# Kernel optimization log

Measured on AMD Instinct MI355X. Metric: run time of the kernel, lower is better.

Reference implementation:

```python
import jax, jax.numpy as jnp
import numpy as np

B, L, D = 2, 2048, 1024
H = 16          # num_heads == num_key_value_heads
FD = 16         # feature_dim (q/k head dim)
HD = D // H     # head_dim = 64 (v head dim)
EPS = 1e-5


def setup_inputs() -> dict:
    key = jax.random.key(0)
    k0, k1, k2, k3, k4 = jax.random.split(key, 5)
    scale = 0.02
    return {
        "hidden_states": jax.random.normal(k0, (B, L, D), jnp.float32),
        "Wq": jax.random.normal(k1, (D, H * FD), jnp.float32) * scale,
        "Wk": jax.random.normal(k2, (D, H * FD), jnp.float32) * scale,
        "Wv": jax.random.normal(k3, (D, H * HD), jnp.float32) * scale,
        "Wo": jax.random.normal(k4, (H * HD, D), jnp.float32) * scale,
    }


def reference(hidden_states, Wq, Wk, Wv, Wo):
    # projections (bias-free), split heads: b l (h d) -> b h l d
    q = (hidden_states @ Wq).reshape(B, L, H, FD).transpose(0, 2, 1, 3)
    k = (hidden_states @ Wk).reshape(B, L, H, FD).transpose(0, 2, 1, 3)
    v = (hidden_states @ Wv).reshape(B, L, H, HD).transpose(0, 2, 1, 3)

    # parallel_rebased: squared-dot-product kernel attention, causal,
    # row-normalized by the kernel sum (use_scale=True, use_normalize=True)
    qk_scale = FD ** -0.5
    s = jnp.einsum('bhqd,bhkd->bhqk', q * qk_scale, k)
    s = s * s  # quadratic feature map: (q.k)^2
    causal = jnp.tril(jnp.ones((L, L), dtype=bool))
    s = jnp.where(causal, s, 0.0)
    z = jnp.sum(s, axis=-1)  # [B,H,L]
    o = jnp.einsum('bhqk,bhkd->bhqd', s, v) / (z[..., None] + EPS)

    # merge heads: b h l d -> b l (h d), output projection
    o = o.transpose(0, 2, 1, 3).reshape(B, L, H * HD)
    return o @ Wo
```

## Files before the change

kernel.cpp:

```cpp
#include <hip/hip_runtime.h>
#include <hip/hip_bf16.h>

#define BB 2
#define LL 2048
#define DD 1024
#define HH 16
#define FD 16
#define HD 64
#define EPS 1e-5f
#define RQKV 1536
#define NFIX 4

typedef __attribute__((ext_vector_type(4))) float f32x4;
typedef __attribute__((ext_vector_type(8))) _Float16 f16x8;
typedef __attribute__((ext_vector_type(4))) _Float16 f16x4;

__global__ __launch_bounds__(256) void transpose_cast(
    const float* __restrict__ src, _Float16* __restrict__ dst, int K, int N) {
  __shared__ _Float16 s[32][40];
  const int n0 = blockIdx.x * 32, k0 = blockIdx.y * 32;
  const int tid = threadIdx.x;
  {
    int r = tid >> 3, c = (tid & 7) * 4;
    float4 v = *(const float4*)(src + (size_t)(k0 + r) * N + n0 + c);
    f16x4 p = {(_Float16)v.x, (_Float16)v.y, (_Float16)v.z, (_Float16)v.w};
    *(f16x4*)&s[r][c] = p;
  }
  __syncthreads();
  {
    int n = tid >> 3, kk = (tid & 7) * 4;
    f16x4 o = {s[kk + 0][n], s[kk + 1][n], s[kk + 2][n], s[kk + 3][n]};
    *(f16x4*)(dst + (size_t)(n0 + n) * K + k0 + kk) = o;
  }
}

template <typename AT, typename OutT>
__global__ __launch_bounds__(256) void gemm_tn(
    const AT* __restrict__ A, const _Float16* __restrict__ Bt,
    OutT* __restrict__ C, int M, int N, int K) {
  constexpr int LDT = 40;
  __shared__ __attribute__((aligned(16))) _Float16 sA[128 * LDT];
  __shared__ __attribute__((aligned(16))) _Float16 sB[128 * LDT];
  const int tid = threadIdx.x;
  const int m0 = blockIdx.y * 128, n0 = blockIdx.x * 128;
  const int w = tid >> 6, lane = tid & 63, quad = lane >> 4, l16 = lane & 15;
  const int wm = (w >> 1) * 64, wn = (w & 1) * 64;

  const int sr = tid >> 1, sh = (tid & 1) * 16;
  const AT* Ag = A + (size_t)(m0 + sr) * K + sh;
  const _Float16* Bg = Bt + (size_t)(n0 + sr) * K + sh;
  _Float16* sAw = &sA[sr * LDT + sh];
  _Float16* sBw = &sB[sr * LDT + sh];

  f32x4 acc[4][4];
#pragma unroll
  for (int i = 0; i < 4; i++)
#pragma unroll
    for (int j = 0; j < 4; j++) acc[i][j] = (f32x4){0.f, 0.f, 0.f, 0.f};

  float4 ar32[4];
  f16x8 ar16[2];
  f16x8 br[2];
  auto LOAD = [&](int k0) {
    if constexpr (sizeof(AT) == 4) {
      ar32[0] = *(const float4*)(Ag + k0);
      ar32[1] = *(const float4*)(Ag + k0 + 4);
      ar32[2] = *(const float4*)(Ag + k0 + 8);
      ar32[3] = *(const float4*)(Ag + k0 + 12);
    } else {
      ar16[0] = *(const f16x8*)(Ag + k0);
      ar16[1] = *(const f16x8*)(Ag + k0 + 8);
    }
    br[0] = *(const f16x8*)(Bg + k0);
    br[1] = *(const f16x8*)(Bg + k0 + 8);
  };
  LOAD(0);

  for (int k0 = 0; k0 < K; k0 += 32) {
    __syncthreads();
    if constexpr (sizeof(AT) == 4) {
      f16x8 p0 = {(_Float16)ar32[0].x, (_Float16)ar32[0].y, (_Float16)ar32[0].z, (_Float16)ar32[0].w,
                  (_Float16)ar32[1].x, (_Float16)ar32[1].y, (_Float16)ar32[1].z, (_Float16)ar32[1].w};
      f16x8 p1 = {(_Float16)ar32[2].x, (_Float16)ar32[2].y, (_Float16)ar32[2].z, (_Float16)ar32[2].w,
                  (_Float16)ar32[3].x, (_Float16)ar32[3].y, (_Float16)ar32[3].z, (_Float16)ar32[3].w};
      *(f16x8*)sAw = p0;
      *(f16x8*)(sAw + 8) = p1;
    } else {
      *(f16x8*)sAw = ar16[0];
      *(f16x8*)(sAw + 8) = ar16[1];
    }
    *(f16x8*)sBw = br[0];
    *(f16x8*)(sBw + 8) = br[1];
    __syncthreads();
    if (k0 + 32 < K) LOAD(k0 + 32);

    f16x8 af[4], bf[4];
#pragma unroll
    for (int i = 0; i < 4; i++)
      af[i] = *(const f16x8*)&sA[(wm + i * 16 + l16) * LDT + quad * 8];
#pragma unroll
    for (int j = 0; j < 4; j++)
      bf[j] = *(const f16x8*)&sB[(wn + j * 16 + l16) * LDT + quad * 8];
#pragma unroll
    for (int i = 0; i < 4; i++)
#pragma unroll
      for (int j = 0; j < 4; j++)
        acc[i][j] = __builtin_amdgcn_mfma_f32_16x16x32_f16(af[i], bf[j], acc[i][j], 0, 0, 0);
  }

#pragma unroll
  for (int i = 0; i < 4; i++)
#pragma unroll
    for (int j = 0; j < 4; j++)
#pragma unroll
      for (int r = 0; r < 4; r++) {
        const int row = m0 + wm + i * 16 + quad * 4 + r;
        const int col = n0 + wn + j * 16 + l16;
        C[(size_t)row * N + col] = (OutT)acc[i][j][r];
      }
}

#define SK4 24
#define SV4 88
#define SS4 88

__global__ __launch_bounds__(256) void attn_mfma4(
    const _Float16* __restrict__ QKV, _Float16* __restrict__ O) {
  __shared__ __attribute__((aligned(16))) _Float16 sK[64 * SK4];
  __shared__ __attribute__((aligned(16))) _Float16 sVt[80 * SV4];
  __shared__ __attribute__((aligned(16))) _Float16 sS2[4 * 32 * SS4];

  const int bh = blockIdx.y;
  const int b = bh >> 4, h = bh & 15;
  const int qtA = blockIdx.x;
  const int qtB = 31 - qtA;
  const int tid = threadIdx.x;
  const int w = tid >> 6;
  const int lane = tid & 63;
  const int quad = lane >> 4;
  const int l16 = lane & 15;
  const int gqA = qtA * 64 + w * 16;
  const int gqB = qtB * 64 + w * 16;

  f16x8 qfragA = {}, qfragB = {};
  if (quad < 2) {
    qfragA = *(const f16x8*)(QKV +
        (size_t)(b * LL + gqA + l16) * RQKV + h * FD + quad * 8);
    qfragB = *(const f16x8*)(QKV +
        (size_t)(b * LL + gqB + l16) * RQKV + h * FD + quad * 8);
  }

  for (int t = tid; t < 16 * SV4; t += 256) {
    int r = t / SV4, c = t % SV4;
    sVt[64 * SV4 + t] = (_Float16)((r == 0 && c < 64) ? 1.0f : 0.0f);
  }
  __syncthreads();
  const f16x8 zf0 = *(const f16x8*)&sVt[(64 + l16) * SV4 + quad * 8];
  const f16x8 zf1 = *(const f16x8*)&sVt[(64 + l16) * SV4 + 32 + quad * 8];

  f32x4 oaccA[4], oaccB[4];
  f32x4 zaccA = (f32x4){0.f, 0.f, 0.f, 0.f};
  f32x4 zaccB = (f32x4){0.f, 0.f, 0.f, 0.f};
#pragma unroll
  for (int nt = 0; nt < 4; nt++) {
    oaccA[nt] = (f32x4){0.f, 0.f, 0.f, 0.f};
    oaccB[nt] = (f32x4){0.f, 0.f, 0.f, 0.f};
  }

  _Float16* sS2B = sS2 + w * 32 * SS4;
  _Float16* sS2A = sS2B + 16 * SS4;

  const int ktiles = qtB + 1;

  const int skey = tid >> 2, sfg = (tid & 3) * 4;
  uint2 kreg;
  f16x8 vreg0, vreg1;
  auto LOAD = [&](int kt) {
    kreg = *(const uint2*)(QKV +
        (size_t)(b * LL + kt * 64 + skey) * RQKV + 256 + h * FD + sfg);
    const _Float16* vp = QKV +
        (size_t)(b * LL + kt * 64 + lane) * RQKV + 512 + h * HD + w * 16;
    vreg0 = *(const f16x8*)vp;
    vreg1 = *(const f16x8*)(vp + 8);
  };
  LOAD(0);

  for (int kt = 0; kt < ktiles; kt++) {
    __syncthreads();
    *(uint2*)&sK[skey * SK4 + sfg] = kreg;
#pragma unroll
    for (int t = 0; t < 8; t++) sVt[(w * 16 + t) * SV4 + lane] = vreg0[t];
#pragma unroll
    for (int t = 0; t < 8; t++) sVt[(w * 16 + 8 + t) * SV4 + lane] = vreg1[t];
    __syncthreads();
    if (kt + 1 < ktiles) LOAD(kt + 1);

    const int k0 = kt * 64;
    const bool activeA = (kt <= qtA);

    f16x8 kf[4];
#pragma unroll
    for (int nt = 0; nt < 4; nt++) {
      f16x8 f = {};
      if (quad < 2) f = *(const f16x8*)&sK[(nt * 16 + l16) * SK4 + quad * 8];
      kf[nt] = f;
    }

    {
      const bool mask = (kt == qtB);
#pragma unroll
      for (int nt = 0; nt < 4; nt++) {
        f32x4 s = __builtin_amdgcn_mfma_f32_16x16x32_f16(
            qfragB, kf[nt], (f32x4){0.f, 0.f, 0.f, 0.f}, 0, 0, 0);
        const int gk = k0 + nt * 16 + l16;
#pragma unroll
        for (int r = 0; r < 4; r++) {
          float sv = s[r] * s[r] * 2.0f;
          if (mask) sv = (gk <= gqB + quad * 4 + r) ? sv : 0.0f;
          sS2B[(quad * 4 + r) * SS4 + nt * 16 + l16] = (_Float16)sv;
        }
      }
    }
    if (activeA) {
      const bool mask = (kt == qtA);
#pragma unroll
      for (int nt = 0; nt < 4; nt++) {
        f32x4 s = __builtin_amdgcn_mfma_f32_16x16x32_f16(
            qfragA, kf[nt], (f32x4){0.f, 0.f, 0.f, 0.f}, 0, 0, 0);
        const int gk = k0 + nt * 16 + l16;
#pragma unroll
        for (int r = 0; r < 4; r++) {
          float sv = s[r] * s[r] * 2.0f;
          if (mask) sv = (gk <= gqA + quad * 4 + r) ? sv : 0.0f;
          sS2A[(quad * 4 + r) * SS4 + nt * 16 + l16] = (_Float16)sv;
        }
      }
    }
    __asm__ volatile("s_waitcnt lgkmcnt(0)" ::: "memory");

    f16x8 afB0 = *(const f16x8*)&sS2B[l16 * SS4 + quad * 8];
    f16x8 afB1 = *(const f16x8*)&sS2B[l16 * SS4 + 32 + quad * 8];
    f16x8 afA0 = {}, afA1 = {};
    if (activeA) {
      afA0 = *(const f16x8*)&sS2A[l16 * SS4 + quad * 8];
      afA1 = *(const f16x8*)&sS2A[l16 * SS4 + 32 + quad * 8];
    }

#pragma unroll
    for (int nt = 0; nt < 4; nt++) {
      f16x8 vf0 = *(const f16x8*)&sVt[(nt * 16 + l16) * SV4 + quad * 8];
      f16x8 vf1 = *(const f16x8*)&sVt[(nt * 16 + l16) * SV4 + 32 + quad * 8];
      oaccB[nt] = __builtin_amdgcn_mfma_f32_16x16x32_f16(afB0, vf0, oaccB[nt], 0, 0, 0);
      oaccB[nt] = __builtin_amdgcn_mfma_f32_16x16x32_f16(afB1, vf1, oaccB[nt], 0, 0, 0);
      if (activeA) {
        oaccA[nt] = __builtin_amdgcn_mfma_f32_16x16x32_f16(afA0, vf0, oaccA[nt], 0, 0, 0);
        oaccA[nt] = __builtin_amdgcn_mfma_f32_16x16x32_f16(afA1, vf1, oaccA[nt], 0, 0, 0);
      }
    }
    zaccB = __builtin_amdgcn_mfma_f32_16x16x32_f16(afB0, zf0, zaccB, 0, 0, 0);
    zaccB = __builtin_amdgcn_mfma_f32_16x16x32_f16(afB1, zf1, zaccB, 0, 0, 0);
    if (activeA) {
      zaccA = __builtin_amdgcn_mfma_f32_16x16x32_f16(afA0, zf0, zaccA, 0, 0, 0);
      zaccA = __builtin_amdgcn_mfma_f32_16x16x32_f16(afA1, zf1, zaccA, 0, 0, 0);
    }
  }

  {
    float rz[4];
#pragma unroll
    for (int r = 0; r < 4; r++) {
      float zz = __shfl(zaccB[r], lane & 48);
      rz[r] = 1.0f / (zz + 32.0f * EPS);
    }
#pragma unroll
    for (int nt = 0; nt < 4; nt++)
#pragma unroll
      for (int r = 0; r < 4; r++) {
        const int gq = gqB + quad * 4 + r;
        O[(size_t)(b * LL + gq) * (HH * HD) + h * HD + nt * 16 + l16] =
            (_Float16)(oaccB[nt][r] * rz[r]);
      }
  }
  {
    float rz[4];
#pragma unroll
    for (int r = 0; r < 4; r++) {
      float zz = __shfl(zaccA[r], lane & 48);
      rz[r] = 1.0f / (zz + 32.0f * EPS);
    }
#pragma unroll
    for (int nt = 0; nt < 4; nt++)
#pragma unroll
      for (int r = 0; r < 4; r++) {
        const int gq = gqA + quad * 4 + r;
        O[(size_t)(b * LL + gq) * (HH * HD) + h * HD + nt * 16 + l16] =
            (_Float16)(oaccA[nt][r] * rz[r]);
      }
  }
}

__global__ __launch_bounds__(256) void early_qkv(
    const float* __restrict__ hs, const float* __restrict__ Wq,
    const float* __restrict__ Wk, const float* __restrict__ Wv,
    float* __restrict__ QKVe) {
  __shared__ float sHS[8][DD];
  __shared__ float part[8][8][32];
  const int tid = threadIdx.x;
  const int kg = tid >> 5, c = tid & 31;
  const int c0 = blockIdx.x * 32;

  for (int i = tid; i < 8 * (DD / 4); i += 256) {
    int e = i / (DD / 4), col4 = (i % (DD / 4)) * 4;
    int b = e >> 2, r = e & 3;
    *(float4*)&sHS[e][col4] =
        *(const float4*)(hs + (size_t)(b * LL + r) * DD + col4);
  }
  __syncthreads();

  const float* W;
  int col, ncol;
  if (c0 < 256) { W = Wq; col = c0 + c; ncol = 256; }
  else if (c0 < 512) { W = Wk; col = (c0 - 256) + c; ncol = 256; }
  else { W = Wv; col = (c0 - 512) + c; ncol = 1024; }

  float acc[8] = {};
  const int d0 = kg * 128;
#pragma unroll 4
  for (int d = d0; d < d0 + 128; d++) {
    float wv = W[(size_t)d * ncol + col];
#pragma unroll
    for (int e = 0; e < 8; e++) acc[e] += sHS[e][d] * wv;
  }
#pragma unroll
  for (int e = 0; e < 8; e++) part[kg][e][c] = acc[e];
  __syncthreads();

  {
    int e = tid >> 5;
    float t = 0.f;
#pragma unroll
    for (int g = 0; g < 8; g++) t += part[g][e][c];
    QKVe[(size_t)e * RQKV + c0 + c] = t;
  }
}

__global__ __launch_bounds__(256) void fix_final(
    const float* __restrict__ QKVe, _Float16* __restrict__ Oatt) {
  const int b = blockIdx.x >> 4, h = blockIdx.x & 15;
  const int tid = threadIdx.x;
  const int p = tid >> 6, d = tid & 63;

  float num = 0.f, z = 0.f;
  const float* qrow = QKVe + (size_t)(b * 4 + p) * RQKV + h * FD;
  for (int j = 0; j <= p; j++) {
    const float* krow = QKVe + (size_t)(b * 4 + j) * RQKV + 256 + h * FD;
    float s = 0.f;
#pragma unroll
    for (int f = 0; f < FD; f++) s += qrow[f] * krow[f];
    s *= 0.25f;
    s = s * s;
    z += s;
    num += s * QKVe[(size_t)(b * 4 + j) * RQKV + 512 + h * HD + d];
  }
  Oatt[(size_t)(b * LL + p) * (HH * HD) + h * HD + d] =
      (_Float16)(num / (z + EPS));
}

extern "C" void kernel_launch(void* const* d_in, const int* in_sizes, int n_in,
                              void* d_out, int out_size, void* d_ws, size_t ws_size,
                              hipStream_t stream) {
  const float* hs = (const float*)d_in[0];
  const float* Wq = (const float*)d_in[1];
  const float* Wk = (const float*)d_in[2];
  const float* Wv = (const float*)d_in[3];
  const float* Wo = (const float*)d_in[4];
  float* out = (float*)d_out;

  char* ws = (char*)d_ws;
  _Float16* WqkvT = (_Float16*)ws;
  _Float16* WoT   = (_Float16*)(ws + (3ull << 20));
  _Float16* QKV   = (_Float16*)(ws + (8ull << 20));
  _Float16* Oatt  = (_Float16*)(ws + (20ull << 20));
  float*    QKVe  = (float*)(ws + (28ull << 20));

  const int M = BB * LL;

  transpose_cast<<<dim3(256 / 32, DD / 32), 256, 0, stream>>>(Wq, WqkvT, DD, 256);
  transpose_cast<<<dim3(256 / 32, DD / 32), 256, 0, stream>>>(Wk, WqkvT + 256 * DD, DD, 256);
  transpose_cast<<<dim3(DD / 32, DD / 32), 256, 0, stream>>>(Wv, WqkvT + 512 * DD, DD, DD);
  transpose_cast<<<dim3(DD / 32, DD / 32), 256, 0, stream>>>(Wo, WoT, DD, DD);

  early_qkv<<<dim3(RQKV / 32), 256, 0, stream>>>(hs, Wq, Wk, Wv, QKVe);

  gemm_tn<float, _Float16><<<dim3(RQKV / 128, M / 128), 256, 0, stream>>>(
      hs, WqkvT, QKV, M, RQKV, DD);

  attn_mfma4<<<dim3(LL / 128, BB * HH), 256, 0, stream>>>(QKV, Oatt);

  fix_final<<<dim3(BB * HH), 256, 0, stream>>>(QKVe, Oatt);

  gemm_tn<_Float16, float><<<dim3(DD / 128, M / 128), 256, 0, stream>>>(
      Oatt, WoT, out, M, DD, DD);
}
```

Before: 189.0 us.

## Pre-cast hidden states to fp16, merge QKV weight transposes, deepen GEMM K-tile to 64

Adds a separate kernel that converts hidden_states to fp16 once, so the QKV GEMM reads half-width input instead of converting fp32 inside its main loop. The three Q/K/V weight transpose launches are merged into one kernel. The GEMM K-tile grows from 32 to 64, with padded shared-memory rows, which halves the number of loop iterations and barriers. The cost is an extra pass over the activations and about twice the shared memory per block, which may reduce occupancy.

```diff
diff --git a/kernel.cpp b/kernel.cpp
--- a/kernel.cpp
+++ b/kernel.cpp
@@ -15,6 +15,46 @@
 typedef __attribute__((ext_vector_type(8))) _Float16 f16x8;
 typedef __attribute__((ext_vector_type(4))) _Float16 f16x4;
 
+__global__ __launch_bounds__(256) void cast_hs(
+    const float* __restrict__ src, _Float16* __restrict__ dst, int n) {
+  int idx = (blockIdx.x * 256 + threadIdx.x) * 16;
+  if (idx >= n) return;
+#pragma unroll
+  for (int half = 0; half < 2; half++) {
+    float4 a = *(const float4*)(src + idx + half * 8);
+    float4 b = *(const float4*)(src + idx + half * 8 + 4);
+    f16x8 p = {(_Float16)a.x, (_Float16)a.y, (_Float16)a.z, (_Float16)a.w,
+               (_Float16)b.x, (_Float16)b.y, (_Float16)b.z, (_Float16)b.w};
+    *(f16x8*)(dst + idx + half * 8) = p;
+  }
+}
+
+__global__ __launch_bounds__(256) void transpose_qkv(
+    const float* __restrict__ Wq, const float* __restrict__ Wk,
+    const float* __restrict__ Wv, _Float16* __restrict__ dst) {
+  __shared__ _Float16 s[32][40];
+  const int ct = blockIdx.x % 48, kt = blockIdx.x / 48;
+  const float* src;
+  int n0, ncol, drow;
+  if (ct < 8) { src = Wq; n0 = ct * 32; ncol = 256; drow = n0; }
+  else if (ct < 16) { src = Wk; n0 = (ct - 8) * 32; ncol = 256; drow = 256 + n0; }
+  else { src = Wv; n0 = (ct - 16) * 32; ncol = 1024; drow = 512 + n0; }
+  const int k0 = kt * 32;
+  const int tid = threadIdx.x;
+  {
+    int r = tid >> 3, c = (tid & 7) * 4;
+    float4 v = *(const float4*)(src + (size_t)(k0 + r) * ncol + n0 + c);
+    f16x4 p = {(_Float16)v.x, (_Float16)v.y, (_Float16)v.z, (_Float16)v.w};
+    *(f16x4*)&s[r][c] = p;
+  }
+  __syncthreads();
+  {
+    int n = tid >> 3, kk = (tid & 7) * 4;
+    f16x4 o = {s[kk + 0][n], s[kk + 1][n], s[kk + 2][n], s[kk + 3][n]};
+    *(f16x4*)(dst + (size_t)(drow + n) * DD + k0 + kk) = o;
+  }
+}
+
 __global__ __launch_bounds__(256) void transpose_cast(
     const float* __restrict__ src, _Float16* __restrict__ dst, int K, int N) {
   __shared__ _Float16 s[32][40];
@@ -34,11 +74,11 @@
   }
 }
 
-template <typename AT, typename OutT>
-__global__ __launch_bounds__(256) void gemm_tn(
-    const AT* __restrict__ A, const _Float16* __restrict__ Bt,
+template <typename OutT>
+__global__ __launch_bounds__(256) void gemm_f16(
+    const _Float16* __restrict__ A, const _Float16* __restrict__ Bt,
     OutT* __restrict__ C, int M, int N, int K) {
-  constexpr int LDT = 40;
+  constexpr int LDT = 72;
   __shared__ __attribute__((aligned(16))) _Float16 sA[128 * LDT];
   __shared__ __attribute__((aligned(16))) _Float16 sB[128 * LDT];
   const int tid = threadIdx.x;
@@ -46,8 +86,8 @@
   const int w = tid >> 6, lane = tid & 63, quad = lane >> 4, l16 = lane & 15;
   const int wm = (w >> 1) * 64, wn = (w & 1) * 64;
 
-  const int sr = tid >> 1, sh = (tid & 1) * 16;
-  const AT* Ag = A + (size_t)(m0 + sr) * K + sh;
+  const int sr = tid >> 1, sh = (tid & 1) * 32;
+  const _Float16* Ag = A + (size_t)(m0 + sr) * K + sh;
   const _Float16* Bg = Bt + (size_t)(n0 + sr) * K + sh;
   _Float16* sAw = &sA[sr * LDT + sh];
   _Float16* sBw = &sB[sr * LDT + sh];
@@ -58,54 +98,41 @@
 #pragma unroll
     for (int j = 0; j < 4; j++) acc[i][j] = (f32x4){0.f, 0.f, 0.f, 0.f};
 
-  float4 ar32[4];
-  f16x8 ar16[2];
-  f16x8 br[2];
+  f16x8 ar[4], br[4];
   auto LOAD = [&](int k0) {
-    if constexpr (sizeof(AT) == 4) {
-      ar32[0] = *(const float4*)(Ag + k0);
-      ar32[1] = *(const float4*)(Ag + k0 + 4);
-      ar32[2] = *(const float4*)(Ag + k0 + 8);
-      ar32[3] = *(const float4*)(Ag + k0 + 12);
-    } else {
-      ar16[0] = *(const f16x8*)(Ag + k0);
-      ar16[1] = *(const f16x8*)(Ag + k0 + 8);
-    }
-    br[0] = *(const f16x8*)(Bg + k0);
-    br[1] = *(const f16x8*)(Bg + k0 + 8);
+#pragma unroll
+    for (int i = 0; i < 4; i++) {
+      ar[i] = *(const f16x8*)(Ag + k0 + i * 8);
+      br[i] = *(const f16x8*)(Bg + k0 + i * 8);
+    }
   };
   LOAD(0);
 
-  for (int k0 = 0; k0 < K; k0 += 32) {
+  for (int k0 = 0; k0 < K; k0 += 64) {
     __syncthreads();
-    if constexpr (sizeof(AT) == 4) {
-      f16x8 p0 = {(_Float16)ar32[0].x, (_Float16)ar32[0].y, (_Float16)ar32[0].z, (_Float16)ar32[0].w,
-                  (_Float16)ar32[1].x, (_Float16)ar32[1].y, (_Float16)ar32[1].z, (_Float16)ar32[1].w};
-      f16x8 p1 = {(_Float16)ar32[2].x, (_Float16)ar32[2].y, (_Float16)ar32[2].z, (_Float16)ar32[2].w,
-                  (_Float16)ar32[3].x, (_Float16)ar32[3].y, (_Float16)ar32[3].z, (_Float16)ar32[3].w};
-      *(f16x8*)sAw = p0;
-      *(f16x8*)(sAw + 8) = p1;
-    } else {
-      *(f16x8*)sAw = ar16[0];
-      *(f16x8*)(sAw + 8) = ar16[1];
-    }
-    *(f16x8*)sBw = br[0];
-    *(f16x8*)(sBw + 8) = br[1];
+#pragma unroll
+    for (int i = 0; i < 4; i++) {
+      *(f16x8*)(sAw + i * 8) = ar[i];
+      *(f16x8*)(sBw + i * 8) = br[i];
+    }
     __syncthreads();
-    if (k0 + 32 < K) LOAD(k0 + 32);
-
-    f16x8 af[4], bf[4];
-#pragma unroll
-    for (int i = 0; i < 4; i++)
-      af[i] = *(const f16x8*)&sA[(wm + i * 16 + l16) * LDT + quad * 8];
-#pragma unroll
-    for (int j = 0; j < 4; j++)
-      bf[j] = *(const f16x8*)&sB[(wn + j * 16 + l16) * LDT + quad * 8];
-#pragma unroll
-    for (int i = 0; i < 4; i++)
+    if (k0 + 64 < K) LOAD(k0 + 64);
+
+#pragma unroll
+    for (int s = 0; s < 2; s++) {
+      f16x8 af[4], bf[4];
+#pragma unroll
+      for (int i = 0; i < 4; i++)
+        af[i] = *(const f16x8*)&sA[(wm + i * 16 + l16) * LDT + s * 32 + quad * 8];
 #pragma unroll
       for (int j = 0; j < 4; j++)
-        acc[i][j] = __builtin_amdgcn_mfma_f32_16x16x32_f16(af[i], bf[j], acc[i][j], 0, 0, 0);
+        bf[j] = *(const f16x8*)&sB[(wn + j * 16 + l16) * LDT + s * 32 + quad * 8];
+#pragma unroll
+      for (int i = 0; i < 4; i++)
+#pragma unroll
+        for (int j = 0; j < 4; j++)
+          acc[i][j] = __builtin_amdgcn_mfma_f32_16x16x32_f16(af[i], bf[j], acc[i][j], 0, 0, 0);
+    }
   }
 
 #pragma unroll
@@ -379,26 +406,26 @@
   char* ws = (char*)d_ws;
   _Float16* WqkvT = (_Float16*)ws;
   _Float16* WoT   = (_Float16*)(ws + (3ull << 20));
-  _Float16* QKV   = (_Float16*)(ws + (8ull << 20));
-  _Float16* Oatt  = (_Float16*)(ws + (20ull << 20));
-  float*    QKVe  = (float*)(ws + (28ull << 20));
+  _Float16* HS16  = (_Float16*)(ws + (5ull << 20));
+  _Float16* QKV   = (_Float16*)(ws + (13ull << 20));
+  _Float16* Oatt  = (_Float16*)(ws + (25ull << 20));
+  float*    QKVe  = (float*)(ws + (33ull << 20));
 
   const int M = BB * LL;
 
-  transpose_cast<<<dim3(256 / 32, DD / 32), 256, 0, stream>>>(Wq, WqkvT, DD, 256);
-  transpose_cast<<<dim3(256 / 32, DD / 32), 256, 0, stream>>>(Wk, WqkvT + 256 * DD, DD, 256);
-  transpose_cast<<<dim3(DD / 32, DD / 32), 256, 0, stream>>>(Wv, WqkvT + 512 * DD, DD, DD);
+  cast_hs<<<dim3(M * DD / (256 * 16)), 256, 0, stream>>>(hs, HS16, M * DD);
+  transpose_qkv<<<dim3(48 * 32), 256, 0, stream>>>(Wq, Wk, Wv, WqkvT);
   transpose_cast<<<dim3(DD / 32, DD / 32), 256, 0, stream>>>(Wo, WoT, DD, DD);
 
   early_qkv<<<dim3(RQKV / 32), 256, 0, stream>>>(hs, Wq, Wk, Wv, QKVe);
 
-  gemm_tn<float, _Float16><<<dim3(RQKV / 128, M / 128), 256, 0, stream>>>(
-      hs, WqkvT, QKV, M, RQKV, DD);
+  gemm_f16<_Float16><<<dim3(RQKV / 128, M / 128), 256, 0, stream>>>(
+      HS16, WqkvT, QKV, M, RQKV, DD);
 
   attn_mfma4<<<dim3(LL / 128, BB * HH), 256, 0, stream>>>(QKV, Oatt);
 
   fix_final<<<dim3(BB * HH), 256, 0, stream>>>(QKVe, Oatt);
 
-  gemm_tn<_Float16, float><<<dim3(DD / 128, M / 128), 256, 0, stream>>>(
+  gemm_f16<float><<<dim3(DD / 128, M / 128), 256, 0, stream>>>(
       Oatt, WoT, out, M, DD, DD);
 }
```

Measured after the change: 181.9 us. 1.04x faster.
